# Kernel tuning notes

Measured on AMD Instinct MI355X. Metric: run time of the kernel, lower is better.

## Reference

```python
import jax, jax.numpy as jnp
import numpy as np

B, S, D, F, E, NS, K = 2, 2048, 512, 2048, 8, 2, 2


def setup_inputs() -> dict:
    key = jax.random.key(0)
    ks = jax.random.split(key, 6)
    scale = 0.02

    def p(k, shape):
        return jax.random.normal(k, shape, jnp.float32) * scale

    return {
        "x": jax.random.normal(ks[0], (B, S, D), jnp.float32),
        "gate_w": p(ks[1], (E, D)),
        "gate_b": jnp.zeros((E,), jnp.float32),
        "sw1": p(ks[2], (NS, F, D)),
        "sb1": jnp.zeros((NS, F), jnp.float32),
        "sw2": p(ks[3], (NS, D, F)),
        "sb2": jnp.zeros((NS, D), jnp.float32),
        "rw1": p(ks[4], (E, F, D)),
        "rb1": jnp.zeros((E, F), jnp.float32),
        "rw2": p(ks[5], (E, D, F)),
        "rb2": jnp.zeros((E, D), jnp.float32),
    }


def reference(x, gate_w, gate_b, sw1, sb1, sw2, sb2, rw1, rb1, rw2, rb2):
    b, s, d = x.shape
    t = x.reshape(-1, d)  # [T, D] flatten batch*seq tokens
    T = t.shape[0]

    # ---- shared experts: sum over NS FFNs (GELU exact, matching nn.GELU) ----
    hs = jax.nn.gelu(jnp.einsum('td,nfd->ntf', t, sw1) + sb1[:, None, :],
                     approximate=False)
    shared = jnp.einsum('ntf,ndf->td', hs, sw2) + sb2.sum(axis=0)

    # ---- router: softmax over experts, top-k probs/indices ----
    logits = t @ gate_w.T + gate_b               # [T, E]
    probs = jax.nn.softmax(logits, axis=-1)
    top_v, top_i = jax.lax.top_k(probs, K)       # [T, K]

    # combine weights: cw[t, e] = sum_k top_v[t, k] * (top_i[t, k] == e)
    cw = jnp.zeros_like(probs).at[jnp.arange(T)[:, None], top_i].add(top_v)  # [T, E]

    # ---- routed experts: run each expert FFN over all tokens, combine by cw ----
    # Mathematically identical to the masked gather/scatter loop in the source:
    # tokens with cw[t,e]==0 contribute nothing.
    hr = jax.nn.gelu(jnp.einsum('td,efd->etf', t, rw1) + rb1[:, None, :],
                     approximate=False)          # [E, T, F]
    oe = jnp.einsum('etf,edf->etd', hr, rw2) + rb2[:, None, :]  # [E, T, D]
    routed = jnp.einsum('etd,te->td', oe, cw)    # weighted combine

    return (shared + routed).reshape(b, s, d)
```

## Files before the change

### kernel.cpp

```cpp
#include <hip/hip_runtime.h>
#include <math.h>

typedef unsigned short u16;
typedef __attribute__((ext_vector_type(8))) __bf16 bf16x8;
typedef __attribute__((ext_vector_type(4))) float floatx4;

#define T_TOK 4096
#define DD    512
#define FF    2048
#define EE    8
#define NSH   2

#define BM 128
#define BN 128
#define BK 32
#define LDK 40
#define BT2 64
#define CAP 4096
#define PADF 0x80000000u
#define NSLOT (2 * T_TOK + EE * BM)

__device__ __forceinline__ float bf2f(u16 v) {
  union { unsigned int u; float f; } c; c.u = ((unsigned int)v) << 16; return c.f;
}
__device__ __forceinline__ u16 f2bf(float f) {
  union { float ff; unsigned int u; } c; c.ff = f;
  unsigned int u = c.u;
  u += 0x7fffu + ((u >> 16) & 1u);
  return (u16)(u >> 16);
}
__device__ __forceinline__ float decode(const void* p, size_t idx, int f) {
  return f ? ((const float*)p)[idx] : bf2f(((const u16*)p)[idx]);
}
__device__ __forceinline__ bf16x8 load8(const void* base, size_t idx, int f) {
  if (f) {
    const float* p = (const float*)base + idx;
    float4 a = *(const float4*)p;
    float4 b = *(const float4*)(p + 4);
    union { bf16x8 v; u16 s[8]; } u;
    u.s[0] = f2bf(a.x); u.s[1] = f2bf(a.y); u.s[2] = f2bf(a.z); u.s[3] = f2bf(a.w);
    u.s[4] = f2bf(b.x); u.s[5] = f2bf(b.y); u.s[6] = f2bf(b.z); u.s[7] = f2bf(b.w);
    return u.v;
  }
  return *(const bf16x8*)((const u16*)base + idx);
}
__device__ __forceinline__ void loadf8(const void* p, size_t idx, int f,
                                       float* o) {
  if (f) {
    const float* q = (const float*)p + idx;
    float4 a = *(const float4*)q;
    float4 b = *(const float4*)(q + 4);
    o[0] = a.x; o[1] = a.y; o[2] = a.z; o[3] = a.w;
    o[4] = b.x; o[5] = b.y; o[6] = b.z; o[7] = b.w;
  } else {
    union { bf16x8 v; u16 s[8]; } u;
    u.v = *(const bf16x8*)((const u16*)p + idx);
#pragma unroll
    for (int j = 0; j < 8; ++j) o[j] = bf2f(u.s[j]);
  }
}

__device__ __forceinline__ float fast_gelu(float v) {
  float x  = v * 0.70710678118654752f;
  float ax = fabsf(x);
  float t  = __builtin_amdgcn_rcpf(fmaf(0.3275911f, ax, 1.0f));
  float p  = fmaf(t, 1.061405429f, -1.453152027f);
  p = fmaf(t, p, 1.421413741f);
  p = fmaf(t, p, -0.284496736f);
  p = fmaf(t, p, 0.254829592f);
  p = p * t;
  float e  = __expf(-ax * ax);
  float er = fmaf(-p, e, 1.0f);
  er = (x < 0.f) ? -er : er;
  return 0.5f * v * (1.0f + er);
}

__device__ __forceinline__ void gll16(const void* g, void* l) {
  __builtin_amdgcn_global_load_lds(
      (const __attribute__((address_space(1))) void*)g,
      (__attribute__((address_space(3))) void*)l, 16, 0, 0);
}

#define BK2 64
#define TILEU (BM * BK2)

__device__ __forceinline__ void stage8(
    const u16* gA0, const u16* gA1, const u16* gA2, const u16* gA3,
    const u16* gB0, const u16* gB1, const u16* gB2, const u16* gB3,
    u16* Asb, u16* Bsb, int wave, int k0) {
  gll16(gA0 + k0, Asb + wave * 512);
  gll16(gA1 + k0, Asb + 2048 + wave * 512);
  gll16(gA2 + k0, Asb + 4096 + wave * 512);
  gll16(gA3 + k0, Asb + 6144 + wave * 512);
  gll16(gB0 + k0, Bsb + wave * 512);
  gll16(gB1 + k0, Bsb + 2048 + wave * 512);
  gll16(gB2 + k0, Bsb + 4096 + wave * 512);
  gll16(gB3 + k0, Bsb + 6144 + wave * 512);
}

__device__ __forceinline__ void core128swz(
    const u16* gA0, const u16* gA1, const u16* gA2, const u16* gA3,
    const u16* gB0, const u16* gB1, const u16* gB2, const u16* gB3,
    int K, u16* As, u16* Bs, floatx4 acc[4][4],
    int wave, int wm, int wn, int r, int q) {
  const int rs = r & 7;
  for (int k0 = 0; k0 < K; k0 += BK2) {
    __syncthreads();
    stage8(gA0, gA1, gA2, gA3, gB0, gB1, gB2, gB3, As, Bs, wave, k0);
    __syncthreads();
#pragma unroll
    for (int s = 0; s < 2; ++s) {
      bf16x8 af[4], bfr[4];
#pragma unroll
      for (int mi = 0; mi < 4; ++mi) {
        int R = wm + mi * 16 + r;
        int u = (s * 4 + q) ^ rs;
        af[mi] = *(const bf16x8*)(As + R * 64 + u * 8);
      }
#pragma unroll
      for (int ni = 0; ni < 4; ++ni) {
        int R = wn + ni * 16 + r;
        int u = (s * 4 + q) ^ rs;
        bfr[ni] = *(const bf16x8*)(Bs + R * 64 + u * 8);
      }
#pragma unroll
      for (int mi = 0; mi < 4; ++mi)
#pragma unroll
        for (int ni = 0; ni < 4; ++ni)
          acc[mi][ni] = __builtin_amdgcn_mfma_f32_16x16x32_bf16(
              af[mi], bfr[ni], acc[mi][ni], 0, 0, 0);
    }
  }
}

__device__ __forceinline__ void core128pipe(
    const u16* gA0, const u16* gA1, const u16* gA2, const u16* gA3,
    const u16* gB0, const u16* gB1, const u16* gB2, const u16* gB3,
    int K, u16* As, u16* Bs, floatx4 acc[4][4],
    int wave, int wm, int wn, int r, int q) {
  const int rs = r & 7;
  stage8(gA0, gA1, gA2, gA3, gB0, gB1, gB2, gB3, As, Bs, wave, 0);
  int cur = 0;
  for (int k0 = 0; k0 < K; k0 += BK2) {
    const u16* Ac = As + cur * TILEU;
    const u16* Bc = Bs + cur * TILEU;
    if (k0 + BK2 < K) {
      stage8(gA0, gA1, gA2, gA3, gB0, gB1, gB2, gB3,
             As + (cur ^ 1) * TILEU, Bs + (cur ^ 1) * TILEU, wave, k0 + BK2);
      asm volatile("s_waitcnt vmcnt(8)" ::: "memory");
    } else {
      asm volatile("s_waitcnt vmcnt(0)" ::: "memory");
    }
    __builtin_amdgcn_sched_barrier(0);
    __builtin_amdgcn_s_barrier();
    __builtin_amdgcn_sched_barrier(0);
#pragma unroll
    for (int s = 0; s < 2; ++s) {
      bf16x8 af[4], bfr[4];
#pragma unroll
      for (int mi = 0; mi < 4; ++mi) {
        int R = wm + mi * 16 + r;
        int u = (s * 4 + q) ^ rs;
        af[mi] = *(const bf16x8*)(Ac + R * 64 + u * 8);
      }
#pragma unroll
      for (int ni = 0; ni < 4; ++ni) {
        int R = wn + ni * 16 + r;
        int u = (s * 4 + q) ^ rs;
        bfr[ni] = *(const bf16x8*)(Bc + R * 64 + u * 8);
      }
#pragma unroll
      for (int mi = 0; mi < 4; ++mi)
#pragma unroll
        for (int ni = 0; ni < 4; ++ni)
          acc[mi][ni] = __builtin_amdgcn_mfma_f32_16x16x32_bf16(
              af[mi], bfr[ni], acc[mi][ni], 0, 0, 0);
    }
    __builtin_amdgcn_sched_barrier(0);
    __builtin_amdgcn_s_barrier();
    cur ^= 1;
  }
}

__global__ __launch_bounds__(256) void detect_kernel(
    const void* x, const void* gw, const void* sw1, const void* sw2,
    const void* rw1, const void* rw2, int* flags, int* meta) {
  __shared__ int cnt;
  const void* ptrs[6] = {x, gw, sw1, sw2, rw1, rw2};
  int b = blockIdx.x;
  if (threadIdx.x == 0) cnt = 0;
  __syncthreads();
  const u16* p = (const u16*)ptrs[b];
  int local = 0;
  for (int i = threadIdx.x; i < 4096; i += 256) {
    unsigned ef = (p[i] >> 7) & 0xFFu;
    if (ef >= 0xE0u) ++local;
  }
  if (local) atomicAdd(&cnt, local);
  __syncthreads();
  if (threadIdx.x == 0) {
    int f = (cnt >= 16) ? 1 : 0;
    flags[b] = f;
    if (b == 0) {
      flags[6] = f;
      flags[7] = 0;
    }
  }
  if (b == 0 && meta && threadIdx.x < 24) meta[threadIdx.x] = 0;
}

#define U8_X  (T_TOK * DD / 8)
#define U8_S1 (NSH * FF * DD / 8)
#define U8_R1 (EE * FF * DD / 8)
#define U8_S2 (NSH * DD * FF / 8)
#define U8_R2 (EE * DD * FF / 8)
#define U8_C0 (U8_X)
#define U8_C1 (U8_C0 + U8_S1)
#define U8_C2 (U8_C1 + U8_R1)
#define U8_C3 (U8_C2 + U8_S2)
#define U8_C4 (U8_C3 + U8_R2)
__global__ __launch_bounds__(256) void conv_all(
    const void* __restrict__ x, const void* __restrict__ sw1,
    const void* __restrict__ rw1, const void* __restrict__ sw2,
    const void* __restrict__ rw2, u16* __restrict__ xb,
    u16* __restrict__ s1b, u16* __restrict__ r1b, u16* __restrict__ s2b,
    u16* __restrict__ r2b, const int* __restrict__ flags) {
  size_t u = (size_t)blockIdx.x * 256 + threadIdx.x;
  const void* src; u16* dst; int fi; size_t base;
  if (u < U8_C0)      { src = x;   dst = xb;  fi = 0; base = 0; }
  else if (u < U8_C1) { src = sw1; dst = s1b; fi = 2; base = U8_C0; }
  else if (u < U8_C2) { src = rw1; dst = r1b; fi = 4; base = U8_C1; }
  else if (u < U8_C3) { src = sw2; dst = s2b; fi = 3; base = U8_C2; }
  else                { src = rw2; dst = r2b; fi = 5; base = U8_C3; }
  int f = flags[fi];
  if (!f) return;
  size_t i = (u - base) * 8;
  *(bf16x8*)(dst + i) = load8(src, i, f);
}

__global__ __launch_bounds__(256) void router_v(
    const void* __restrict__ x, const void* __restrict__ gw,
    const u16* __restrict__ gb, const int* __restrict__ flags,
    float* __restrict__ cw, int2* __restrict__ tix) {
  int wave = threadIdx.x >> 6, lane = threadIdx.x & 63;
  int t = blockIdx.x * 4 + wave;
  int fx = flags[0], fg = flags[1];
  float xf[8];
  loadf8(x, (size_t)t * DD + lane * 8, fx, xf);
  float acc[EE];
#pragma unroll
  for (int e = 0; e < EE; ++e) {
    float gf[8];
    loadf8(gw, (size_t)e * DD + lane * 8, fg, gf);
    float a = 0.f;
#pragma unroll
    for (int j = 0; j < 8; ++j) a = fmaf(xf[j], gf[j], a);
    acc[e] = a;
  }
#pragma unroll
  for (int e = 0; e < EE; ++e) {
    float v = acc[e];
#pragma unroll
    for (int off = 32; off > 0; off >>= 1) v += __shfl_xor(v, off, 64);
    acc[e] = v;
  }
  if (lane == 0) {
    float m = -1e30f;
#pragma unroll
    for (int e = 0; e < EE; ++e) {
      acc[e] += bf2f(gb[e]);
      m = fmaxf(m, acc[e]);
    }
    float p[EE], s = 0.f;
#pragma unroll
    for (int e = 0; e < EE; ++e) { p[e] = expf(acc[e] - m); s += p[e]; }
    int i1 = 0;
#pragma unroll
    for (int e = 1; e < EE; ++e) if (p[e] > p[i1]) i1 = e;
    int i2 = (i1 == 0) ? 1 : 0;
#pragma unroll
    for (int e = 0; e < EE; ++e)
      if (e != i1 && p[e] > p[i2]) i2 = e;
    float inv = 1.0f / s;
#pragma unroll
    for (int e = 0; e < EE; ++e)
      cw[t * EE + e] = (e == i1 || e == i2) ? p[e] * inv : 0.0f;
    tix[t] = make_int2(i1, i2);
  }
}

__global__ __launch_bounds__(256) void build_lists(
    const int2* __restrict__ tix, int* __restrict__ meta,
    unsigned* __restrict__ list, int4* __restrict__ srec) {
  int t = blockIdx.x * 256 + threadIdx.x;
  if (t >= T_TOK) return;
  int2 ii = tix[t];
  int p0 = atomicAdd(&meta[ii.x], 1);
  list[(size_t)ii.x * CAP + p0] = (unsigned)t;
  int p1 = atomicAdd(&meta[ii.y], 1);
  list[(size_t)ii.y * CAP + p1] = (unsigned)t;
  srec[t] = make_int4(ii.x, p0, ii.y, p1);
}
__global__ __launch_bounds__(256) void pad_lists(int* meta, unsigned* list) {
  if (threadIdx.x == 0) {
    int off = 0;
    for (int e = 0; e < EE; ++e) {
      int c = meta[e];
      int pc = (c + BM - 1) & ~(BM - 1);
      meta[8 + e] = pc;
      meta[16 + e] = off;
      off += pc;
    }
  }
  __syncthreads();
#pragma unroll
  for (int e = 0; e < EE; ++e) {
    int c = meta[e], pc = meta[8 + e];
    int i = c + threadIdx.x;
    if (i < pc) list[(size_t)e * CAP + i] = PADF;
  }
}


__global__ __launch_bounds__(256) void g1_fused(
    const void* __restrict__ xr, const u16* __restrict__ xb,
    const void* __restrict__ s1r, const u16* __restrict__ s1b,
    const u16* __restrict__ sb1,
    const void* __restrict__ r1r, const u16* __restrict__ r1b,
    const u16* __restrict__ rb1, const unsigned* __restrict__ list,
    const int* __restrict__ meta, const int* __restrict__ flags,
    u16* __restrict__ Hsh, u16* __restrict__ Hrt) {
  const u16* xp  = flags[0] ? xb  : (const u16*)xr;
  const u16* s1p = flags[2] ? s1b : (const u16*)s1r;
  const u16* r1p = flags[4] ? r1b : (const u16*)r1r;

  int z  = blockIdx.z;
  int bm = blockIdx.y * BM;
  int xx = blockIdx.x;

  int tid = threadIdx.x, lane = tid & 63, wave = tid >> 6;
  int wm = (wave >> 1) * 64, wn = (wave & 1) * 64;
  int r = lane & 15, q = lane >> 4;
  const int K = DD;

  int rsub = tid >> 3;
  int us = (tid & 7) ^ (rsub & 7);

  __shared__ u16 As[TILEU];
  __shared__ u16 Bs[TILEU];

  const u16 *gA[4], *gB[4];
  int e = 0, ho = 0, bn;
  if (z < 2) {
    bn = (z * 16 + xx) * BN;
#pragma unroll
    for (int c = 0; c < 4; ++c) {
      gA[c] = xp + (size_t)(bm + c * 32 + rsub) * K + us * 8;
      gB[c] = s1p + (size_t)(bn + c * 32 + rsub) * K + us * 8;
    }
  } else {
    e = z - 2;
    if (bm >= meta[8 + e]) return;
    ho = meta[16 + e];
    bn = xx * BN;
#pragma unroll
    for (int c = 0; c < 4; ++c) {
      unsigned tk = list[(size_t)e * CAP + bm + c * 32 + rsub] & 0x7fffffffu;
      gA[c] = xp + (size_t)tk * K + us * 8;
      gB[c] = r1p + (size_t)e * FF * DD + (size_t)(bn + c * 32 + rsub) * K +
              us * 8;
    }
  }

  floatx4 acc[4][4];
  floatx4 zero = {0.f, 0.f, 0.f, 0.f};
#pragma unroll
  for (int i = 0; i < 4; ++i)
#pragma unroll
    for (int j = 0; j < 4; ++j) acc[i][j] = zero;

  core128swz(gA[0], gA[1], gA[2], gA[3], gB[0], gB[1], gB[2], gB[3],
             K, As, Bs, acc, wave, wm, wn, r, q);

  if (z < 2) {
#pragma unroll
    for (int mi = 0; mi < 4; ++mi)
#pragma unroll
      for (int ni = 0; ni < 4; ++ni) {
        int col = bn + wn + ni * 16 + r;
        float bv = bf2f(sb1[col]);
#pragma unroll
        for (int rr = 0; rr < 4; ++rr) {
          int row = bm + wm + mi * 16 + q * 4 + rr;
          float v = acc[mi][ni][rr] + bv;
          Hsh[(size_t)row * (NSH * FF) + col] = f2bf(fast_gelu(v));
        }
      }
  } else {
#pragma unroll
    for (int mi = 0; mi < 4; ++mi)
#pragma unroll
      for (int ni = 0; ni < 4; ++ni) {
        int col = bn + wn + ni * 16 + r;
        float bv = bf2f(rb1[(size_t)e * FF + col]);
#pragma unroll
        for (int rr = 0; rr < 4; ++rr) {
          int slot = bm + wm + mi * 16 + q * 4 + rr;
          float v = acc[mi][ni][rr] + bv;
          Hrt[(size_t)(ho + slot) * FF + col] = f2bf(fast_gelu(v));
        }
      }
  }
}

__global__ __launch_bounds__(256) void g2_fused(
    const u16* __restrict__ Hsh,
    const void* __restrict__ s2r, const u16* __restrict__ s2b,
    const u16* __restrict__ sb2, const u16* __restrict__ Hrt,
    const void* __restrict__ r2r, const u16* __restrict__ r2b,
    const u16* __restrict__ rb2,
    const unsigned* __restrict__ list, const int* __restrict__ meta,
    const int* __restrict__ flags, const float* __restrict__ cw,
    float* __restrict__ oacc, float* __restrict__ Ort) {
  const u16* s2p = flags[3] ? s2b : (const u16*)s2r;
  const u16* r2p = flags[5] ? r2b : (const u16*)r2r;

  int L  = blockIdx.x + 4 * (blockIdx.y + 32 * blockIdx.z);
  int xx = (L & 31) >> 3;
  int pp = ((L >> 5) << 3) | (L & 7);
  int z  = pp >> 5;
  int bm = (pp & 31) * BM;
  int bn = xx * BN;

  int tid = threadIdx.x, lane = tid & 63, wave = tid >> 6;
  int wm = (wave >> 1) * 64, wn = (wave & 1) * 64;
  int r = lane & 15, q = lane >> 4;
  const int K = FF;

  int rsub = tid >> 3;
  int us = (tid & 7) ^ (rsub & 7);

  __shared__ u16 As[2 * TILEU];
  __shared__ u16 Bs[2 * TILEU];

  const u16 *gA[4], *gB[4];
  int e = 0, ho = 0;
  if (z < NSH) {
    const int ldA = NSH * FF;
#pragma unroll
    for (int c = 0; c < 4; ++c) {
      gA[c] = Hsh + (size_t)(bm + c * 32 + rsub) * ldA + (size_t)z * FF +
              us * 8;
      gB[c] = s2p + (size_t)z * DD * FF + (size_t)(bn + c * 32 + rsub) * K +
              us * 8;
    }
  } else {
    e = z - NSH;
    if (bm >= meta[8 + e]) return;
    ho = meta[16 + e];
#pragma unroll
    for (int c = 0; c < 4; ++c) {
      gA[c] = Hrt + (size_t)(ho + bm + c * 32 + rsub) * K + us * 8;
      gB[c] = r2p + (size_t)e * DD * FF + (size_t)(bn + c * 32 + rsub) * K +
              us * 8;
    }
  }

  floatx4 acc[4][4];
  floatx4 zero = {0.f, 0.f, 0.f, 0.f};
#pragma unroll
  for (int i = 0; i < 4; ++i)
#pragma unroll
    for (int j = 0; j < 4; ++j) acc[i][j] = zero;

  core128pipe(gA[0], gA[1], gA[2], gA[3], gB[0], gB[1], gB[2], gB[3],
              K, As, Bs, acc, wave, wm, wn, r, q);

  if (z < NSH) {
    float* op = oacc + (size_t)z * T_TOK * DD;
#pragma unroll
    for (int mi = 0; mi < 4; ++mi)
#pragma unroll
      for (int ni = 0; ni < 4; ++ni) {
        int col = bn + wn + ni * 16 + r;
        float bv = bf2f(sb2[(size_t)z * DD + col]);
#pragma unroll
        for (int rr = 0; rr < 4; ++rr) {
          int row = bm + wm + mi * 16 + q * 4 + rr;
          op[(size_t)row * DD + col] = acc[mi][ni][rr] + bv;
        }
      }
  } else {
#pragma unroll
    for (int mi = 0; mi < 4; ++mi)
#pragma unroll
      for (int rr = 0; rr < 4; ++rr) {
        int slot = bm + wm + mi * 16 + q * 4 + rr;
        unsigned raw = list[(size_t)e * CAP + slot];
        if (raw & PADF) continue;
        float s = cw[raw * EE + e];
#pragma unroll
        for (int ni = 0; ni < 4; ++ni) {
          int col = bn + wn + ni * 16 + r;
          float v = acc[mi][ni][rr] + bf2f(rb2[(size_t)e * DD + col]);
          Ort[(size_t)(ho + slot) * DD + col] = s * v;
        }
      }
  }
}

typedef struct { u16 a, b, c, d; } u16x4;
__global__ __launch_bounds__(256) void combine_out(
    const float* __restrict__ oacc, const float* __restrict__ Ort,
    const int4* __restrict__ srec, const int* __restrict__ meta,
    void* __restrict__ out, const int* __restrict__ flags) {
  int t  = blockIdx.x * 2 + (threadIdx.x >> 7);
  int c4 = (threadIdx.x & 127) * 4;
  int4 sr = srec[t];
  int g0 = meta[16 + sr.x] + sr.y;
  int g1 = meta[16 + sr.z] + sr.w;
  float4 a = *(const float4*)(oacc + (size_t)t * DD + c4);
  float4 b = *(const float4*)(oacc + (size_t)(T_TOK + t) * DD + c4);
  float4 u = *(const float4*)(Ort + (size_t)g0 * DD + c4);
  float4 v = *(const float4*)(Ort + (size_t)g1 * DD + c4);
  float o0 = a.x + b.x + u.x + v.x;
  float o1 = a.y + b.y + u.y + v.y;
  float o2 = a.z + b.z + u.z + v.z;
  float o3 = a.w + b.w + u.w + v.w;
  size_t idx = (size_t)t * DD + c4;
  if (flags[6]) {
    *(float4*)((float*)out + idx) = make_float4(o0, o1, o2, o3);
  } else {
    u16x4 h = {f2bf(o0), f2bf(o1), f2bf(o2), f2bf(o3)};
    *(u16x4*)((u16*)out + idx) = h;
  }
}

__device__ __forceinline__ void gemm_core(const void* A, size_t aoff, int fA,
                                          const void* B, size_t boff, int fB,
                                          int K, u16* As, u16* Bs,
                                          floatx4 acc[4][4]) {
  int tid  = threadIdx.x;
  int lane = tid & 63, wave = tid >> 6;
  int wm = (wave >> 1) * 64, wn = (wave & 1) * 64;
  int r = lane & 15, q = lane >> 4;
  int srow = tid >> 2;
  int sc8  = (tid & 3) * 8;
  size_t abase = aoff + (size_t)srow * K + sc8;
  size_t bbase = boff + (size_t)srow * K + sc8;
  const size_t half = (size_t)64 * K;

  for (int k0 = 0; k0 < K; k0 += BK) {
    bf16x8 av0 = load8(A, abase + k0, fA);
    bf16x8 av1 = load8(A, abase + half + k0, fA);
    bf16x8 bv0 = load8(B, bbase + k0, fB);
    bf16x8 bv1 = load8(B, bbase + half + k0, fB);
    __syncthreads();
    *(bf16x8*)(As + srow * LDK + sc8)        = av0;
    *(bf16x8*)(As + (srow + 64) * LDK + sc8) = av1;
    *(bf16x8*)(Bs + srow * LDK + sc8)        = bv0;
    *(bf16x8*)(Bs + (srow + 64) * LDK + sc8) = bv1;
    __syncthreads();

    bf16x8 af[4], bfr[4];
#pragma unroll
    for (int mi = 0; mi < 4; ++mi)
      af[mi] = *(const bf16x8*)(As + (wm + mi * 16 + r) * LDK + q * 8);
#pragma unroll
    for (int ni = 0; ni < 4; ++ni)
      bfr[ni] = *(const bf16x8*)(Bs + (wn + ni * 16 + r) * LDK + q * 8);
#pragma unroll
    for (int mi = 0; mi < 4; ++mi)
#pragma unroll
      for (int ni = 0; ni < 4; ++ni)
        acc[mi][ni] = __builtin_amdgcn_mfma_f32_16x16x32_bf16(
            af[mi], bfr[ni], acc[mi][ni], 0, 0, 0);
  }
}

__global__ __launch_bounds__(256) void gemm1_gelu(
    const void* __restrict__ A, size_t aoff, const void* __restrict__ B,
    size_t boff, const u16* __restrict__ bias, size_t bioff,
    u16* __restrict__ H, const int* __restrict__ flags, int iA, int iB,
    int N, int K) {
  __shared__ u16 As[BM * LDK];
  __shared__ u16 Bs[BN * LDK];
  int fA = flags[iA], fB = flags[iB];
  floatx4 acc[4][4];
  floatx4 zero = {0.f, 0.f, 0.f, 0.f};
#pragma unroll
  for (int i = 0; i < 4; ++i)
#pragma unroll
    for (int j = 0; j < 4; ++j) acc[i][j] = zero;

  int bm = blockIdx.y * BM, bn = blockIdx.x * BN;
  gemm_core(A, aoff + (size_t)bm * K, fA, B, boff + (size_t)bn * K, fB, K,
            As, Bs, acc);

  int tid = threadIdx.x, wave = tid >> 6, lane = tid & 63;
  int wm = (wave >> 1) * 64, wn = (wave & 1) * 64;
  int r = lane & 15, q = lane >> 4;
#pragma unroll
  for (int mi = 0; mi < 4; ++mi)
#pragma unroll
    for (int ni = 0; ni < 4; ++ni) {
      int col = bn + wn + ni * 16 + r;
      float bv = bf2f(bias[bioff + col]);
#pragma unroll
      for (int rr = 0; rr < 4; ++rr) {
        int row = bm + wm + mi * 16 + q * 4 + rr;
        float v = acc[mi][ni][rr] + bv;
        H[(size_t)row * N + col] = f2bf(fast_gelu(v));
      }
    }
}

__global__ __launch_bounds__(256) void gemm2_acc(
    const u16* __restrict__ A, const void* __restrict__ B, size_t boff,
    const u16* __restrict__ bias, size_t bioff, float* __restrict__ outf,
    void* __restrict__ outb, const float* __restrict__ cw,
    const int* __restrict__ flags, int iB, int expert, int accum,
    int row0, int N, int K) {
  __shared__ u16 As[BT2 * LDK];
  __shared__ u16 Bs[BT2 * LDK];
  int fB = flags[iB], fO = flags[6];
  floatx4 acc[2][2];
  floatx4 zero = {0.f, 0.f, 0.f, 0.f};
#pragma unroll
  for (int i = 0; i < 2; ++i)
#pragma unroll
    for (int j = 0; j < 2; ++j) acc[i][j] = zero;

  int bm = blockIdx.y * BT2, bn = blockIdx.x * BT2;
  int tid  = threadIdx.x;
  int lane = tid & 63, wave = tid >> 6;
  int wm = (wave >> 1) * 32, wn = (wave & 1) * 32;
  int r = lane & 15, q = lane >> 4;
  int srow = tid >> 2;
  int sc8  = (tid & 3) * 8;
  size_t abase = (size_t)(bm + srow) * K + sc8;
  size_t bbase = boff + (size_t)(bn + srow) * K + sc8;

  for (int k0 = 0; k0 < K; k0 += BK) {
    bf16x8 av = *(const bf16x8*)(A + abase + k0);
    bf16x8 bv = load8(B, bbase + k0, fB);
    __syncthreads();
    *(bf16x8*)(As + srow * LDK + sc8) = av;
    *(bf16x8*)(Bs + srow * LDK + sc8) = bv;
    __syncthreads();

    bf16x8 af[2], bfr[2];
#pragma unroll
    for (int mi = 0; mi < 2; ++mi)
      af[mi] = *(const bf16x8*)(As + (wm + mi * 16 + r) * LDK + q * 8);
#pragma unroll
    for (int ni = 0; ni < 2; ++ni)
      bfr[ni] = *(const bf16x8*)(Bs + (wn + ni * 16 + r) * LDK + q * 8);
#pragma unroll
    for (int mi = 0; mi < 2; ++mi)
#pragma unroll
      for (int ni = 0; ni < 2; ++ni)
        acc[mi][ni] = __builtin_amdgcn_mfma_f32_16x16x32_bf16(
            af[mi], bfr[ni], acc[mi][ni], 0, 0, 0);
  }

#pragma unroll
  for (int mi = 0; mi < 2; ++mi)
#pragma unroll
    for (int rr = 0; rr < 4; ++rr) {
      int grow = row0 + bm + wm + mi * 16 + q * 4 + rr;
      float s = cw ? cw[grow * EE + expert] : 1.0f;
#pragma unroll
      for (int ni = 0; ni < 2; ++ni) {
        int col = bn + wn + ni * 16 + r;
        float v = acc[mi][ni][rr] + bf2f(bias[bioff + col]);
        size_t idx = (size_t)grow * N + col;
        if (outf) {
          float prev = accum ? outf[idx] : 0.0f;
          outf[idx] = prev + s * v;
        } else if (fO) {
          float* ob = (float*)outb;
          float prev = accum ? ob[idx] : 0.0f;
          ob[idx] = prev + s * v;
        } else {
          u16* ob = (u16*)outb;
          float prev = accum ? bf2f(ob[idx]) : 0.0f;
          ob[idx] = f2bf(prev + s * v);
        }
      }
    }
}

__global__ __launch_bounds__(256) void convert_out(
    const float* __restrict__ acc, void* __restrict__ out,
    const int* __restrict__ flags, int n) {
  int i = blockIdx.x * blockDim.x + threadIdx.x;
  if (i >= n) return;
  if (flags[6]) ((float*)out)[i] = acc[i];
  else ((u16*)out)[i] = f2bf(acc[i]);
}

extern "C" void kernel_launch(void* const* d_in, const int* in_sizes, int n_in,
                              void* d_out, int out_size, void* d_ws, size_t ws_size,
                              hipStream_t stream) {
  (void)in_sizes; (void)n_in; (void)out_size;
  const void* x   = d_in[0];
  const void* gw  = d_in[1];
  const u16*  gb  = (const u16*)d_in[2];
  const void* sw1 = d_in[3];
  const u16*  sb1 = (const u16*)d_in[4];
  const void* sw2 = d_in[5];
  const u16*  sb2 = (const u16*)d_in[6];
  const void* rw1 = d_in[7];
  const u16*  rb1 = (const u16*)d_in[8];
  const void* rw2 = d_in[9];
  const u16*  rb2 = (const u16*)d_in[10];

  const size_t NX   = (size_t)T_TOK * DD;
  const size_t NW1S = (size_t)NSH * FF * DD;
  const size_t NW1R = (size_t)EE * FF * DD;
  const size_t NW2S = (size_t)NSH * DD * FF;
  const size_t NW2R = (size_t)EE * DD * FF;

  size_t off = 0;
  const size_t flO   = off; off += 256;
  const size_t cwO   = off; off += (size_t)T_TOK * EE * 4;
  const size_t tixO  = off; off += (size_t)T_TOK * 8;
  const size_t metaO = off; off += 256;
  const size_t listO = off; off += (size_t)EE * CAP * 4;
  const size_t srecO = off; off += (size_t)T_TOK * 16;
  const size_t accO  = off; off += (size_t)NSH * T_TOK * DD * 4;
  const size_t hshO  = off; off += (size_t)T_TOK * NSH * FF * 2;
  const size_t hrtO  = off; off += (size_t)NSLOT * FF * 2;
  const size_t ortO  = off; off += (size_t)NSLOT * DD * 4;
  const size_t xbO   = off; off += NX * 2;
  const size_t s1O   = off; off += NW1S * 2;
  const size_t r1O   = off; off += NW1R * 2;
  const size_t s2O   = off; off += NW2S * 2;
  const size_t r2O   = off; off += NW2R * 2;
  const int fast = (off <= ws_size) ? 1 : 0;

  char* ws = (char*)d_ws;
  int*   flags = (int*)(ws + flO);
  float* cw    = (float*)(ws + cwO);
  dim3 blk(256);

  if (fast) {
    int2*     tix  = (int2*)(ws + tixO);
    int*      meta = (int*)(ws + metaO);
    unsigned* list = (unsigned*)(ws + listO);
    int4*     srec = (int4*)(ws + srecO);
    float*    oacc = (float*)(ws + accO);
    u16*      Hsh  = (u16*)(ws + hshO);
    u16*      Hrt  = (u16*)(ws + hrtO);
    float*    Ort  = (float*)(ws + ortO);
    u16*      xb   = (u16*)(ws + xbO);
    u16*      s1b  = (u16*)(ws + s1O);
    u16*      r1b  = (u16*)(ws + r1O);
    u16*      s2b  = (u16*)(ws + s2O);
    u16*      r2b  = (u16*)(ws + r2O);

    detect_kernel<<<6, 256, 0, stream>>>(x, gw, sw1, sw2, rw1, rw2, flags,
                                         meta);
    conv_all<<<U8_C4 / 256, 256, 0, stream>>>(x, sw1, rw1, sw2, rw2, xb, s1b,
                                              r1b, s2b, r2b, flags);
    router_v<<<T_TOK / 4, 256, 0, stream>>>(x, gw, gb, flags, cw, tix);
    build_lists<<<T_TOK / 256, 256, 0, stream>>>(tix, meta, list, srec);
    pad_lists<<<1, 256, 0, stream>>>(meta, list);

    dim3 gf1(16, T_TOK / BM, 2 + EE);
    g1_fused<<<gf1, blk, 0, stream>>>(x, xb, sw1, s1b, sb1, rw1, r1b, rb1,
                                      list, meta, flags, Hsh, Hrt);
    dim3 gf2(DD / BN, CAP / BM, NSH + EE);
    g2_fused<<<gf2, blk, 0, stream>>>(Hsh, sw2, s2b, sb2, Hrt, rw2, r2b, rb2,
                                      list, meta, flags, cw, oacc, Ort);
    combine_out<<<T_TOK / 2, 256, 0, stream>>>(oacc, Ort, srec, meta, d_out,
                                               flags);
    return;
  }

  detect_kernel<<<6, 256, 0, stream>>>(x, gw, sw1, sw2, rw1, rw2, flags,
                                       nullptr);
  const size_t flB = 256, cwB = (size_t)T_TOK * EE * 4, tixB = (size_t)T_TOK * 8;
  const size_t accB = (size_t)T_TOK * DD * 4;
  static const int tcs[4] = {4096, 2048, 1024, 512};
  int TC = 0, use_f32 = 1;
  for (int i = 0; i < 4; ++i)
    if (flB + cwB + tixB + accB + (size_t)tcs[i] * FF * 2 <= ws_size) { TC = tcs[i]; break; }
  if (!TC) {
    use_f32 = 0;
    for (int i = 0; i < 4; ++i)
      if (flB + cwB + tixB + (size_t)tcs[i] * FF * 2 <= ws_size) { TC = tcs[i]; break; }
  }
  if (!TC) { TC = 512; use_f32 = 0; }

  int2*  tix     = (int2*)(ws + flB + cwB);
  float* out_acc = use_f32 ? (float*)(ws + flB + cwB + tixB) : nullptr;
  u16*   H       = (u16*)(ws + flB + cwB + tixB + (use_f32 ? accB : 0));

  router_v<<<T_TOK / 4, 256, 0, stream>>>(x, gw, gb, flags, cw, tix);
  dim3 g1(FF / BN, TC / BM);
  dim3 g2(DD / BT2, TC / BT2);
  const int nchunk = T_TOK / TC;
  for (int f = 0; f < NSH + EE; ++f) {
    const void *w1, *w2; const u16 *b1, *b2; const float* cwp;
    int expert, i1, i2v; size_t w1off, w2off, b1off, b2off;
    if (f < NSH) {
      w1 = sw1; w2 = sw2; b1 = sb1; b2 = sb2;
      w1off = (size_t)f * FF * DD; w2off = (size_t)f * DD * FF;
      b1off = (size_t)f * FF; b2off = (size_t)f * DD;
      cwp = nullptr; expert = 0; i1 = 2; i2v = 3;
    } else {
      int e = f - NSH;
      w1 = rw1; w2 = rw2; b1 = rb1; b2 = rb2;
      w1off = (size_t)e * FF * DD; w2off = (size_t)e * DD * FF;
      b1off = (size_t)e * FF; b2off = (size_t)e * DD;
      cwp = cw; expert = e; i1 = 4; i2v = 5;
    }
    int accum = (f > 0) ? 1 : 0;
    for (int c = 0; c < nchunk; ++c) {
      size_t t0 = (size_t)c * TC;
      gemm1_gelu<<<g1, blk, 0, stream>>>(x, t0 * DD, w1, w1off, b1, b1off, H,
                                         flags, 0, i1, FF, DD);
      gemm2_acc<<<g2, blk, 0, stream>>>(H, w2, w2off, b2, b2off, out_acc,
                                        d_out, cwp, flags, i2v, expert, accum,
                                        (int)t0, DD, FF);
    }
  }
  if (use_f32)
    convert_out<<<(T_TOK * DD) / 256, 256, 0, stream>>>(out_acc, d_out, flags,
                                                        T_TOK * DD);
}
```

Before: 336.0 us.

## Run first fused GEMM with 8 waves per 128x128 tile

The first-layer fused GEMM kernel (shared and routed experts) now launches 512 threads per block instead of 256. Each of the 8 waves computes a 32x64 sub-tile with a 2x4 accumulator array instead of 64x64 with 4x4, and each wave stages two A rows and two B rows per k-step. The inlined loop replaces the removed core128swz helper. This is meant to raise latency hiding and occupancy per CU while lowering per-thread register pressure, at the cost of more synchronisation participants and less fragment reuse per wave.

```diff
diff --git a/kernel.cpp b/kernel.cpp
--- a/kernel.cpp
+++ b/kernel.cpp
@@ -96,41 +96,6 @@
   gll16(gB1 + k0, Bsb + 2048 + wave * 512);
   gll16(gB2 + k0, Bsb + 4096 + wave * 512);
   gll16(gB3 + k0, Bsb + 6144 + wave * 512);
-}
-
-__device__ __forceinline__ void core128swz(
-    const u16* gA0, const u16* gA1, const u16* gA2, const u16* gA3,
-    const u16* gB0, const u16* gB1, const u16* gB2, const u16* gB3,
-    int K, u16* As, u16* Bs, floatx4 acc[4][4],
-    int wave, int wm, int wn, int r, int q) {
-  const int rs = r & 7;
-  for (int k0 = 0; k0 < K; k0 += BK2) {
-    __syncthreads();
-    stage8(gA0, gA1, gA2, gA3, gB0, gB1, gB2, gB3, As, Bs, wave, k0);
-    __syncthreads();
-#pragma unroll
-    for (int s = 0; s < 2; ++s) {
-      bf16x8 af[4], bfr[4];
-#pragma unroll
-      for (int mi = 0; mi < 4; ++mi) {
-        int R = wm + mi * 16 + r;
-        int u = (s * 4 + q) ^ rs;
-        af[mi] = *(const bf16x8*)(As + R * 64 + u * 8);
-      }
-#pragma unroll
-      for (int ni = 0; ni < 4; ++ni) {
-        int R = wn + ni * 16 + r;
-        int u = (s * 4 + q) ^ rs;
-        bfr[ni] = *(const bf16x8*)(Bs + R * 64 + u * 8);
-      }
-#pragma unroll
-      for (int mi = 0; mi < 4; ++mi)
-#pragma unroll
-        for (int ni = 0; ni < 4; ++ni)
-          acc[mi][ni] = __builtin_amdgcn_mfma_f32_16x16x32_bf16(
-              af[mi], bfr[ni], acc[mi][ni], 0, 0, 0);
-    }
-  }
 }
 
 __device__ __forceinline__ void core128pipe(
@@ -322,7 +287,7 @@
 }
 
 
-__global__ __launch_bounds__(256) void g1_fused(
+__global__ __launch_bounds__(512) void g1_fused(
     const void* __restrict__ xr, const u16* __restrict__ xb,
     const void* __restrict__ s1r, const u16* __restrict__ s1b,
     const u16* __restrict__ sb1,
@@ -339,52 +304,83 @@
   int xx = blockIdx.x;
 
   int tid = threadIdx.x, lane = tid & 63, wave = tid >> 6;
-  int wm = (wave >> 1) * 64, wn = (wave & 1) * 64;
+  int wm = (wave & 3) * 32;
+  int wn = (wave >> 2) * 64;
   int r = lane & 15, q = lane >> 4;
   const int K = DD;
 
-  int rsub = tid >> 3;
-  int us = (tid & 7) ^ (rsub & 7);
+  int lrow = lane >> 3;
+  int us = (lane & 7) ^ lrow;
 
   __shared__ u16 As[TILEU];
   __shared__ u16 Bs[TILEU];
 
-  const u16 *gA[4], *gB[4];
+  const u16 *gA0, *gA1, *gB0, *gB1;
   int e = 0, ho = 0, bn;
   if (z < 2) {
     bn = (z * 16 + xx) * BN;
-#pragma unroll
-    for (int c = 0; c < 4; ++c) {
-      gA[c] = xp + (size_t)(bm + c * 32 + rsub) * K + us * 8;
-      gB[c] = s1p + (size_t)(bn + c * 32 + rsub) * K + us * 8;
-    }
+    gA0 = xp + (size_t)(bm + wave * 16 + lrow) * K + us * 8;
+    gA1 = xp + (size_t)(bm + wave * 16 + 8 + lrow) * K + us * 8;
+    gB0 = s1p + (size_t)(bn + wave * 16 + lrow) * K + us * 8;
+    gB1 = s1p + (size_t)(bn + wave * 16 + 8 + lrow) * K + us * 8;
   } else {
     e = z - 2;
     if (bm >= meta[8 + e]) return;
     ho = meta[16 + e];
     bn = xx * BN;
-#pragma unroll
-    for (int c = 0; c < 4; ++c) {
-      unsigned tk = list[(size_t)e * CAP + bm + c * 32 + rsub] & 0x7fffffffu;
-      gA[c] = xp + (size_t)tk * K + us * 8;
-      gB[c] = r1p + (size_t)e * FF * DD + (size_t)(bn + c * 32 + rsub) * K +
-              us * 8;
-    }
-  }
-
-  floatx4 acc[4][4];
+    unsigned t0 = list[(size_t)e * CAP + bm + wave * 16 + lrow] & 0x7fffffffu;
+    unsigned t1 =
+        list[(size_t)e * CAP + bm + wave * 16 + 8 + lrow] & 0x7fffffffu;
+    gA0 = xp + (size_t)t0 * K + us * 8;
+    gA1 = xp + (size_t)t1 * K + us * 8;
+    gB0 = r1p + (size_t)e * FF * DD + (size_t)(bn + wave * 16 + lrow) * K +
+          us * 8;
+    gB1 = r1p + (size_t)e * FF * DD +
+          (size_t)(bn + wave * 16 + 8 + lrow) * K + us * 8;
+  }
+
+  floatx4 acc[2][4];
   floatx4 zero = {0.f, 0.f, 0.f, 0.f};
 #pragma unroll
-  for (int i = 0; i < 4; ++i)
+  for (int i = 0; i < 2; ++i)
 #pragma unroll
     for (int j = 0; j < 4; ++j) acc[i][j] = zero;
 
-  core128swz(gA[0], gA[1], gA[2], gA[3], gB[0], gB[1], gB[2], gB[3],
-             K, As, Bs, acc, wave, wm, wn, r, q);
+  const int rs = r & 7;
+  for (int k0 = 0; k0 < K; k0 += BK2) {
+    __syncthreads();
+    gll16(gA0 + k0, As + wave * 1024);
+    gll16(gA1 + k0, As + wave * 1024 + 512);
+    gll16(gB0 + k0, Bs + wave * 1024);
+    gll16(gB1 + k0, Bs + wave * 1024 + 512);
+    __syncthreads();
+#pragma unroll
+    for (int s = 0; s < 2; ++s) {
+      bf16x8 af[2], bfr[4];
+#pragma unroll
+      for (int mi = 0; mi < 2; ++mi) {
+        int R = wm + mi * 16 + r;
+        int u = (s * 4 + q) ^ rs;
+        af[mi] = *(const bf16x8*)(As + R * 64 + u * 8);
+      }
+#pragma unroll
+      for (int ni = 0; ni < 4; ++ni) {
+        int R = wn + ni * 16 + r;
+        int u = (s * 4 + q) ^ rs;
+        bfr[ni] = *(const bf16x8*)(Bs + R * 64 + u * 8);
+      }
+#pragma unroll
+      for (int mi = 0; mi < 2; ++mi)
+#pragma unroll
+        for (int ni = 0; ni < 4; ++ni)
+          acc[mi][ni] = __builtin_amdgcn_mfma_f32_16x16x32_bf16(
+              af[mi], bfr[ni], acc[mi][ni], 0, 0, 0);
+    }
+  }
 
   if (z < 2) {
 #pragma unroll
-    for (int mi = 0; mi < 4; ++mi)
+    for (int mi = 0; mi < 2; ++mi)
 #pragma unroll
       for (int ni = 0; ni < 4; ++ni) {
         int col = bn + wn + ni * 16 + r;
@@ -398,7 +394,7 @@
       }
   } else {
 #pragma unroll
-    for (int mi = 0; mi < 4; ++mi)
+    for (int mi = 0; mi < 2; ++mi)
 #pragma unroll
       for (int ni = 0; ni < 4; ++ni) {
         int col = bn + wn + ni * 16 + r;
@@ -769,8 +765,8 @@
     pad_lists<<<1, 256, 0, stream>>>(meta, list);
 
     dim3 gf1(16, T_TOK / BM, 2 + EE);
-    g1_fused<<<gf1, blk, 0, stream>>>(x, xb, sw1, s1b, sb1, rw1, r1b, rb1,
-                                      list, meta, flags, Hsh, Hrt);
+    g1_fused<<<gf1, dim3(512), 0, stream>>>(x, xb, sw1, s1b, sb1, rw1, r1b,
+                                            rb1, list, meta, flags, Hsh, Hrt);
     dim3 gf2(DD / BN, CAP / BM, NSH + EE);
     g2_fused<<<gf2, blk, 0, stream>>>(Hsh, sw2, s2b, sb2, Hrt, rw2, r2b, rb2,
                                       list, meta, flags, cw, oacc, Ort);
```

Result: faster. 326.9 us (-2.7%).
